# Kernel tuning notes

Measured on AMD Instinct MI355X. Metric: run time of the kernel, lower is better.

## Reference

```python
import jax, jax.numpy as jnp
import numpy as np

D = 768

def setup_inputs() -> dict:
    key = jax.random.key(0)
    k1, k2, k3, k4, k5 = jax.random.split(key, 5)
    B, C, Q = 32, 512, 128
    cont_embs = jax.random.normal(k1, (B, C, D), dtype=jnp.float32)
    ques_embs = jax.random.normal(k2, (B, Q, D), dtype=jnp.float32)
    cont_masks = jax.random.randint(k3, (B, C), 0, 2, dtype=jnp.int32)
    ques_masks = jax.random.randint(k4, (B, Q), 0, 2, dtype=jnp.int32)
    # S_W param, 'uniform' initializer (keras default: U[-0.05, 0.05])
    S_W = jax.random.uniform(k5, (3 * D,), dtype=jnp.float32, minval=-0.05, maxval=0.05)
    return {"cont_embs": cont_embs, "cont_masks": cont_masks,
            "ques_embs": ques_embs, "ques_masks": ques_masks, "S_W": S_W}

def reference(cont_embs, cont_masks, ques_embs, ques_masks, S_W):
    c, q = cont_embs, ques_embs          # (B,C,D), (B,Q,D)
    # Decompose reduce_sum(concat([c_tile, q_tile, c*q], -1) * S_W, -1)
    # into rank-1 bias terms + a single matmul (no (B,C,Q,3D) materialization).
    w1, w2, w3 = S_W[:D], S_W[D:2 * D], S_W[2 * D:]
    similarity = (jnp.einsum('bcd,d->bc', c, w1)[:, :, None]
                  + jnp.einsum('bqd,d->bq', q, w2)[:, None, :]
                  + jnp.einsum('bcd,bqd->bcq', c * w3, q))   # (B,C,Q)
    NEG = jnp.float32(-1e30)
    exp_mask_c2q = (1.0 - ques_masks.astype(jnp.float32))[:, None, :] * NEG  # (B,1,Q)
    # NOTE: original code applies softmax over axis=1 (context axis), faithfully kept.
    c2q_dist = jax.nn.softmax(similarity + exp_mask_c2q, axis=1)  # (B,C,Q)
    c2q = jnp.einsum('bcq,bqd->bcd', c2q_dist, q)                 # (B,C,D)
    S_max = jnp.max(similarity, axis=2)                           # (B,C)
    exp_mask_S = (1.0 - cont_masks.astype(jnp.float32)) * NEG     # (B,C)
    c_dash_dist = jax.nn.softmax(S_max + exp_mask_S, axis=1)      # (B,C)
    c_dash = jnp.einsum('bc,bcd->bd', c_dash_dist, c)[:, None, :] # (B,1,D)
    c_c2q = c * c2q
    c_c_dash = c * c_dash
    attn_output = jnp.concatenate([c2q, c_c2q, c_c_dash], axis=2)  # (B,C,3D)
    # dropout omitted (deterministic reference)
    blended_reps = jnp.concatenate([c, attn_output], axis=2)       # (B,C,4D)
    return blended_reps
```

## Files before the change

kernel.cpp:

```cpp
#include <hip/hip_runtime.h>
#include <hip/hip_bf16.h>

#define B_ 32
#define C_ 512
#define Q_ 128
#define D_ 768
constexpr float NEGV = -1e30f;
constexpr float CINV = 1.0f / 512.0f;

typedef short bf16x8 __attribute__((ext_vector_type(8)));
typedef short bf16x4 __attribute__((ext_vector_type(4)));
typedef float f32x4 __attribute__((ext_vector_type(4)));

__device__ __forceinline__ short f2bf(float x) {
    union { float f; unsigned u; } v; v.f = x;
    unsigned r = v.u + 0x7fffu + ((v.u >> 16) & 1u);
    return (short)(r >> 16);
}

__global__ void k_dots(const float* __restrict__ cont, const float* __restrict__ ques,
                       const float* __restrict__ SW, float* __restrict__ cdot,
                       float* __restrict__ qdot) {
    int w = threadIdx.x >> 6;
    int lane = threadIdx.x & 63;
    int r = blockIdx.x * 4 + w;
    const float* row;
    const float* wv;
    if (r < B_ * C_) { row = cont + (size_t)r * D_; wv = SW; }
    else             { row = ques + (size_t)(r - B_ * C_) * D_; wv = SW + D_; }
    float s = 0.f;
#pragma unroll
    for (int i = 0; i < D_ / 64; ++i) {
        int d = lane + i * 64;
        s += row[d] * wv[d];
    }
#pragma unroll
    for (int off = 32; off; off >>= 1) s += __shfl_xor(s, off, 64);
    if (lane == 0) {
        if (r < B_ * C_) cdot[r] = s;
        else qdot[r - B_ * C_] = s;
    }
}

__global__ void __launch_bounds__(512) k_sim(const float* __restrict__ cont,
                                             const float* __restrict__ ques,
                                             const float* __restrict__ SW,
                                             const float* __restrict__ cdot,
                                             const float* __restrict__ qdot,
                                             float* __restrict__ S,
                                             float* __restrict__ Smax) {
    const int b = blockIdx.y, c0 = blockIdx.x * 64;
    __shared__ short Alds[64 * 32];
    __shared__ short Blds[128 * 32];
    __shared__ float rowpart[4][64];
    char* Ab = (char*)Alds;
    char* Bb = (char*)Blds;
    const int t = threadIdx.x;
    const int w = t >> 6, l = t & 63;
    const int woffm = (w >> 2) * 32, woffn = (w & 3) * 32;
    const int lhi = l >> 4, llo = l & 15;
    f32x4 acc[2][2] = {};

    const int arow = t >> 3, akq = (t & 7) * 4;
    const int brow = t >> 2, bkq = (t & 3) * 8;
    const float* Ap = cont + ((size_t)(b * C_ + c0 + arow)) * D_ + akq;
    const float* Bp = ques + ((size_t)(b * Q_ + brow)) * D_ + bkq;
    const float* w3 = SW + 2 * D_;
    const int aoff = arow * 64 + ((((akq >> 3) ^ (arow & 3)) << 4) | ((akq & 4) << 1));
    const int boff = brow * 64 + (((bkq >> 3) ^ (brow & 3)) << 4);

    for (int k0 = 0; k0 < D_; k0 += 32) {
        float4 av = *(const float4*)(Ap + k0);
        float4 w4 = *(const float4*)(w3 + k0 + akq);
        bf16x4 a4;
        a4[0] = f2bf(av.x * w4.x); a4[1] = f2bf(av.y * w4.y);
        a4[2] = f2bf(av.z * w4.z); a4[3] = f2bf(av.w * w4.w);
        *(bf16x4*)(Ab + aoff) = a4;
        float4 b0 = *(const float4*)(Bp + k0);
        float4 b1 = *(const float4*)(Bp + k0 + 4);
        bf16x8 b8;
        b8[0] = f2bf(b0.x); b8[1] = f2bf(b0.y); b8[2] = f2bf(b0.z); b8[3] = f2bf(b0.w);
        b8[4] = f2bf(b1.x); b8[5] = f2bf(b1.y); b8[6] = f2bf(b1.z); b8[7] = f2bf(b1.w);
        *(bf16x8*)(Bb + boff) = b8;
        __syncthreads();
        bf16x8 af[2], bfv[2];
#pragma unroll
        for (int mi = 0; mi < 2; ++mi) {
            int row = woffm + mi * 16 + llo;
            af[mi] = *(bf16x8*)(Ab + row * 64 + ((lhi ^ (row & 3)) << 4));
        }
#pragma unroll
        for (int ni = 0; ni < 2; ++ni) {
            int row = woffn + ni * 16 + llo;
            bfv[ni] = *(bf16x8*)(Bb + row * 64 + ((lhi ^ (row & 3)) << 4));
        }
#pragma unroll
        for (int mi = 0; mi < 2; ++mi)
#pragma unroll
            for (int ni = 0; ni < 2; ++ni)
                acc[mi][ni] = __builtin_amdgcn_mfma_f32_16x16x32_bf16(af[mi], bfv[ni], acc[mi][ni], 0, 0, 0);
        __syncthreads();
    }

    float qd0 = qdot[b * Q_ + woffn + llo];
    float qd1 = qdot[b * Q_ + woffn + 16 + llo];
#pragma unroll
    for (int mi = 0; mi < 2; ++mi) {
#pragma unroll
        for (int i = 0; i < 4; ++i) {
            int cl = woffm + mi * 16 + lhi * 4 + i;
            float cd = cdot[b * C_ + c0 + cl];
            size_t srow = ((size_t)(b * C_ + c0 + cl)) * Q_;
            float v0 = acc[mi][0][i] + cd + qd0;
            float v1 = acc[mi][1][i] + cd + qd1;
            S[srow + woffn + llo] = v0;
            S[srow + woffn + 16 + llo] = v1;
            float vm = fmaxf(v0, v1);
#pragma unroll
            for (int off = 1; off < 16; off <<= 1) vm = fmaxf(vm, __shfl_xor(vm, off, 64));
            if (llo == 0) rowpart[w & 3][cl] = vm;
        }
    }
    __syncthreads();
    if (t < 64) {
        float m = fmaxf(fmaxf(rowpart[0][t], rowpart[1][t]), fmaxf(rowpart[2][t], rowpart[3][t]));
        Smax[b * C_ + c0 + t] = m;
    }
}

__global__ void k_colstats(const float* __restrict__ S, float* __restrict__ colM,
                           float* __restrict__ colInvL) {
    int b = blockIdx.y;
    int ql = threadIdx.x & 31;
    int q = blockIdx.x * 32 + ql;
    int strip = threadIdx.x >> 5;
    float m = -INFINITY, l = 0.f;
    const float* Sp = S + ((size_t)(b * C_ + strip * 64)) * Q_ + q;
    for (int c = 0; c < 64; ++c) {
        float v = Sp[(size_t)c * Q_];
        if (v > m) { l = l * __expf(m - v) + 1.f; m = v; }
        else l += __expf(v - m);
    }
    __shared__ float sm[8][32], sl[8][32];
    sm[strip][ql] = m; sl[strip][ql] = l;
    __syncthreads();
    if (threadIdx.x < 32) {
        float M = sm[0][ql], L = sl[0][ql];
#pragma unroll
        for (int i = 1; i < 8; ++i) {
            float mi = sm[i][ql], li = sl[i][ql];
            if (mi > M) { L = L * __expf(M - mi) + li; M = mi; }
            else L += li * __expf(mi - M);
        }
        colM[b * Q_ + q] = M;
        colInvL[b * Q_ + q] = 1.f / L;
    }
}

__global__ void k_cdash(const float* __restrict__ cont, const int* __restrict__ cmask,
                        const float* __restrict__ Smax, float* __restrict__ cdash) {
    int b = blockIdx.y, d0 = blockIdx.x * 64;
    __shared__ float dist[C_];
    __shared__ float red[256];
    __shared__ float ps[4][64];
    int t = threadIdx.x;
    float v0 = Smax[b * C_ + t]       + (cmask[b * C_ + t]       ? 0.f : NEGV);
    float v1 = Smax[b * C_ + t + 256] + (cmask[b * C_ + t + 256] ? 0.f : NEGV);
    float m = fmaxf(v0, v1);
    red[t] = m; __syncthreads();
    for (int s = 128; s; s >>= 1) { if (t < s) red[t] = fmaxf(red[t], red[t + s]); __syncthreads(); }
    m = red[0]; __syncthreads();
    float e0 = __expf(v0 - m), e1 = __expf(v1 - m);
    red[t] = e0 + e1; __syncthreads();
    for (int s = 128; s; s >>= 1) { if (t < s) red[t] += red[t + s]; __syncthreads(); }
    float inv = 1.f / red[0];
    dist[t] = e0 * inv; dist[t + 256] = e1 * inv;
    __syncthreads();
    int d = d0 + (t & 63), strip = t >> 6;
    float acc = 0.f;
    const float* cp = cont + ((size_t)(b * C_ + strip * 128)) * D_ + d;
#pragma unroll 4
    for (int c = 0; c < 128; ++c) acc += dist[strip * 128 + c] * cp[(size_t)c * D_];
    ps[strip][t & 63] = acc;
    __syncthreads();
    if (t < 64) cdash[b * D_ + d0 + t] = ps[0][t] + ps[1][t] + ps[2][t] + ps[3][t];
}

__global__ void __launch_bounds__(256) k_final(const float* __restrict__ cont,
                                               const float* __restrict__ ques,
                                               const int* __restrict__ qmask,
                                               const float* __restrict__ S,
                                               const float* __restrict__ colM,
                                               const float* __restrict__ colInvL,
                                               const float* __restrict__ cdash,
                                               float* __restrict__ out) {
    const int b = blockIdx.z, c0 = blockIdx.x * 64, D0 = blockIdx.y * 64;
    __shared__ short Alds[64 * 32];
    __shared__ short BldsT[64 * 32];
    __shared__ float colMl[Q_];
    __shared__ float scl[Q_];
    __shared__ float Cf[64][68];
    char* Ab = (char*)Alds;
    char* Bb = (char*)BldsT;
    const int t = threadIdx.x;
    const int w = t >> 6, l = t & 63;
    const int woffm = (w >> 1) * 32, woffn = (w & 1) * 32;
    const int lhi = l >> 4, llo = l & 15;
    f32x4 acc[2][2] = {};

    if (t < Q_) {
        colMl[t] = colM[b * Q_ + t];
        scl[t] = qmask[b * Q_ + t] ? colInvL[b * Q_ + t] : -1.f;
    }
    __syncthreads();

    const int arow = t >> 2, akq = (t & 3) * 8;
    const int qloc = t & 31, dgrp = t >> 5;
    const int aoff = arow * 64 + (((akq >> 3) ^ (arow & 3)) << 4);

    for (int kk = 0; kk < 4; ++kk) {
        const int q0 = kk * 32;
        {
            const float* sp = S + ((size_t)(b * C_ + c0 + arow)) * Q_ + q0 + akq;
            float4 s0 = *(const float4*)sp;
            float4 s1 = *(const float4*)(sp + 4);
            float sv[8] = {s0.x, s0.y, s0.z, s0.w, s1.x, s1.y, s1.z, s1.w};
            bf16x8 a8;
#pragma unroll
            for (int j = 0; j < 8; ++j) {
                int q = q0 + akq + j;
                float sc = scl[q];
                float dist = (sc < 0.f) ? CINV : __expf(sv[j] - colMl[q]) * sc;
                a8[j] = f2bf(dist);
            }
            *(bf16x8*)(Ab + aoff) = a8;
        }
        {
            const float* qp = ques + ((size_t)(b * Q_ + q0 + qloc)) * D_ + D0 + dgrp * 8;
            float4 b0 = *(const float4*)qp;
            float4 b1 = *(const float4*)(qp + 4);
            float bv[8] = {b0.x, b0.y, b0.z, b0.w, b1.x, b1.y, b1.z, b1.w};
#pragma unroll
            for (int j = 0; j < 8; ++j) {
                int d = dgrp * 8 + j;
                int byte = d * 64 + ((((qloc >> 3) ^ (d & 3)) << 4) | ((qloc & 7) * 2));
                *(short*)(Bb + byte) = f2bf(bv[j]);
            }
        }
        __syncthreads();
        bf16x8 af[2], bfv[2];
#pragma unroll
        for (int mi = 0; mi < 2; ++mi) {
            int row = woffm + mi * 16 + llo;
            af[mi] = *(bf16x8*)(Ab + row * 64 + ((lhi ^ (row & 3)) << 4));
        }
#pragma unroll
        for (int ni = 0; ni < 2; ++ni) {
            int row = woffn + ni * 16 + llo;
            bfv[ni] = *(bf16x8*)(Bb + row * 64 + ((lhi ^ (row & 3)) << 4));
        }
#pragma unroll
        for (int mi = 0; mi < 2; ++mi)
#pragma unroll
            for (int ni = 0; ni < 2; ++ni)
                acc[mi][ni] = __builtin_amdgcn_mfma_f32_16x16x32_bf16(af[mi], bfv[ni], acc[mi][ni], 0, 0, 0);
        __syncthreads();
    }

#pragma unroll
    for (int mi = 0; mi < 2; ++mi)
#pragma unroll
        for (int ni = 0; ni < 2; ++ni)
#pragma unroll
            for (int i = 0; i < 4; ++i)
                Cf[woffm + mi * 16 + lhi * 4 + i][woffn + ni * 16 + llo] = acc[mi][ni][i];
    __syncthreads();

    const int r = t >> 2, dch = (t & 3) * 16;
    const int cg = c0 + r;
    const float* cp = cont + ((size_t)(b * C_ + cg)) * D_ + D0 + dch;
    const float* dp = cdash + b * D_ + D0 + dch;
    float* op = out + ((size_t)(b * C_ + cg)) * (size_t)(4 * D_) + D0 + dch;
#pragma unroll
    for (int j = 0; j < 4; ++j) {
        float4 cv = *(const float4*)(cp + 4 * j);
        float4 av = *(const float4*)&Cf[r][dch + 4 * j];
        float4 dv = *(const float4*)(dp + 4 * j);
        float4 m1 = {cv.x * av.x, cv.y * av.y, cv.z * av.z, cv.w * av.w};
        float4 m2 = {cv.x * dv.x, cv.y * dv.y, cv.z * dv.z, cv.w * dv.w};
        *(float4*)(op + 4 * j) = cv;
        *(float4*)(op + D_ + 4 * j) = av;
        *(float4*)(op + 2 * D_ + 4 * j) = m1;
        *(float4*)(op + 3 * D_ + 4 * j) = m2;
    }
}

extern "C" void kernel_launch(void* const* d_in, const int* in_sizes, int n_in,
                              void* d_out, int out_size, void* d_ws, size_t ws_size,
                              hipStream_t stream) {
    const float* cont  = (const float*)d_in[0];
    const int*   cmask = (const int*)d_in[1];
    const float* ques  = (const float*)d_in[2];
    const int*   qmask = (const int*)d_in[3];
    const float* SW    = (const float*)d_in[4];
    float* out = (float*)d_out;

    float* ws      = (float*)d_ws;
    float* S       = ws;
    float* Smax    = S + (size_t)B_ * C_ * Q_;
    float* colM    = Smax + B_ * C_;
    float* colInvL = colM + B_ * Q_;
    float* cdot    = colInvL + B_ * Q_;
    float* qdot    = cdot + B_ * C_;
    float* cdash   = qdot + B_ * Q_;

    k_dots<<<(B_ * C_ + B_ * Q_) / 4, 256, 0, stream>>>(cont, ques, SW, cdot, qdot);
    k_sim<<<dim3(C_ / 64, B_), 512, 0, stream>>>(cont, ques, SW, cdot, qdot, S, Smax);
    k_colstats<<<dim3(Q_ / 32, B_), 256, 0, stream>>>(S, colM, colInvL);
    k_cdash<<<dim3(D_ / 64, B_), 256, 0, stream>>>(cont, cmask, Smax, cdash);
    k_final<<<dim3(C_ / 64, D_ / 64, B_), 256, 0, stream>>>(cont, ques, qmask, S, colM, colInvL, cdash, out);
}
```

Before: 358.4 us.

## Precompute bf16 operands and softmax dist, feed MFMA directly from global memory

Adds a prep kernel that writes a bf16 copy of cont*w3 and of ques while computing the rank-1 dots, a transpose kernel for ques, and a separate kernel that turns S into bf16 softmax weights. The sim and final GEMMs then load MFMA fragments straight from global memory, with no LDS staging, no conversions and no barriers in the K loop. Column stats and the sim kernel also use smaller blocks so more of them run at once. The aim is to stop redoing fp32-to-bf16 conversion and exp work in every tile, at the price of extra workspace traffic and more kernel launches.

New measurement: 322.2 us. -10.1%, faster.

```diff
diff --git a/kernel.cpp b/kernel.cpp
--- a/kernel.cpp
+++ b/kernel.cpp
@@ -18,143 +18,170 @@
     return (short)(r >> 16);
 }
 
-__global__ void k_dots(const float* __restrict__ cont, const float* __restrict__ ques,
-                       const float* __restrict__ SW, float* __restrict__ cdot,
+__global__ void k_prep(const float* __restrict__ cont, const float* __restrict__ ques,
+                       const float* __restrict__ SW, short* __restrict__ contw3,
+                       short* __restrict__ quesbf, float* __restrict__ cdot,
                        float* __restrict__ qdot) {
-    int w = threadIdx.x >> 6;
     int lane = threadIdx.x & 63;
-    int r = blockIdx.x * 4 + w;
-    const float* row;
-    const float* wv;
-    if (r < B_ * C_) { row = cont + (size_t)r * D_; wv = SW; }
-    else             { row = ques + (size_t)(r - B_ * C_) * D_; wv = SW + D_; }
-    float s = 0.f;
-#pragma unroll
-    for (int i = 0; i < D_ / 64; ++i) {
-        int d = lane + i * 64;
-        s += row[d] * wv[d];
-    }
-#pragma unroll
-    for (int off = 32; off; off >>= 1) s += __shfl_xor(s, off, 64);
-    if (lane == 0) {
-        if (r < B_ * C_) cdot[r] = s;
-        else qdot[r - B_ * C_] = s;
-    }
-}
-
-__global__ void __launch_bounds__(512) k_sim(const float* __restrict__ cont,
-                                             const float* __restrict__ ques,
-                                             const float* __restrict__ SW,
+    int r = blockIdx.x * 4 + (threadIdx.x >> 6);
+    float acc = 0.f;
+    if (r < B_ * C_) {
+        const float* row = cont + (size_t)r * D_;
+        short* orow = contw3 + (size_t)r * D_;
+#pragma unroll
+        for (int i = 0; i < 3; ++i) {
+            int k = i * 256 + lane * 4;
+            float4 f = *(const float4*)(row + k);
+            float4 a = *(const float4*)(SW + k);
+            float4 m = *(const float4*)(SW + 2 * D_ + k);
+            acc += f.x * a.x + f.y * a.y + f.z * a.z + f.w * a.w;
+            bf16x4 p;
+            p[0] = f2bf(f.x * m.x); p[1] = f2bf(f.y * m.y);
+            p[2] = f2bf(f.z * m.z); p[3] = f2bf(f.w * m.w);
+            *(bf16x4*)(orow + k) = p;
+        }
+#pragma unroll
+        for (int off = 32; off; off >>= 1) acc += __shfl_xor(acc, off, 64);
+        if (lane == 0) cdot[r] = acc;
+    } else {
+        int r2 = r - B_ * C_;
+        const float* row = ques + (size_t)r2 * D_;
+        short* orow = quesbf + (size_t)r2 * D_;
+#pragma unroll
+        for (int i = 0; i < 3; ++i) {
+            int k = i * 256 + lane * 4;
+            float4 f = *(const float4*)(row + k);
+            float4 a = *(const float4*)(SW + D_ + k);
+            acc += f.x * a.x + f.y * a.y + f.z * a.z + f.w * a.w;
+            bf16x4 p;
+            p[0] = f2bf(f.x); p[1] = f2bf(f.y); p[2] = f2bf(f.z); p[3] = f2bf(f.w);
+            *(bf16x4*)(orow + k) = p;
+        }
+#pragma unroll
+        for (int off = 32; off; off >>= 1) acc += __shfl_xor(acc, off, 64);
+        if (lane == 0) qdot[r2] = acc;
+    }
+}
+
+__global__ void k_qt(const short* __restrict__ quesbf, short* __restrict__ quesT) {
+    const int d0 = blockIdx.x * 64, q0 = blockIdx.y * 64, b = blockIdx.z;
+    __shared__ short T[64][65];
+    const int t = threadIdx.x;
+#pragma unroll
+    for (int p = 0; p < 2; ++p) {
+        int ql = p * 32 + (t >> 3), dl = (t & 7) * 8;
+        bf16x8 v = *(const bf16x8*)(quesbf + ((size_t)(b * Q_ + q0 + ql)) * D_ + d0 + dl);
+#pragma unroll
+        for (int j = 0; j < 8; ++j) T[ql][dl + j] = v[j];
+    }
+    __syncthreads();
+#pragma unroll
+    for (int p = 0; p < 2; ++p) {
+        int dl = p * 32 + (t >> 3), ql = (t & 7) * 8;
+        bf16x8 v;
+#pragma unroll
+        for (int j = 0; j < 8; ++j) v[j] = T[ql + j][dl];
+        *(bf16x8*)(quesT + ((size_t)(b * D_ + d0 + dl)) * Q_ + q0 + ql) = v;
+    }
+}
+
+__global__ void __launch_bounds__(256) k_sim(const short* __restrict__ contw3,
+                                             const short* __restrict__ quesbf,
                                              const float* __restrict__ cdot,
                                              const float* __restrict__ qdot,
                                              float* __restrict__ S,
                                              float* __restrict__ Smax) {
-    const int b = blockIdx.y, c0 = blockIdx.x * 64;
-    __shared__ short Alds[64 * 32];
-    __shared__ short Blds[128 * 32];
-    __shared__ float rowpart[4][64];
-    char* Ab = (char*)Alds;
-    char* Bb = (char*)Blds;
-    const int t = threadIdx.x;
-    const int w = t >> 6, l = t & 63;
-    const int woffm = (w >> 2) * 32, woffn = (w & 3) * 32;
-    const int lhi = l >> 4, llo = l & 15;
+    const int b = blockIdx.y, c0 = blockIdx.x * 32;
+    const int t = threadIdx.x, w = t >> 6, l = t & 63;
+    const int llo = l & 15, lhi = l >> 4;
+    __shared__ float rowpart[4][32];
+    const short* Ab = contw3 + ((size_t)(b * C_ + c0)) * D_ + lhi * 8;
+    const short* Bb = quesbf + ((size_t)(b * Q_ + w * 32)) * D_ + lhi * 8;
     f32x4 acc[2][2] = {};
-
-    const int arow = t >> 3, akq = (t & 7) * 4;
-    const int brow = t >> 2, bkq = (t & 3) * 8;
-    const float* Ap = cont + ((size_t)(b * C_ + c0 + arow)) * D_ + akq;
-    const float* Bp = ques + ((size_t)(b * Q_ + brow)) * D_ + bkq;
-    const float* w3 = SW + 2 * D_;
-    const int aoff = arow * 64 + ((((akq >> 3) ^ (arow & 3)) << 4) | ((akq & 4) << 1));
-    const int boff = brow * 64 + (((bkq >> 3) ^ (brow & 3)) << 4);
-
+#pragma unroll 4
     for (int k0 = 0; k0 < D_; k0 += 32) {
-        float4 av = *(const float4*)(Ap + k0);
-        float4 w4 = *(const float4*)(w3 + k0 + akq);
-        bf16x4 a4;
-        a4[0] = f2bf(av.x * w4.x); a4[1] = f2bf(av.y * w4.y);
-        a4[2] = f2bf(av.z * w4.z); a4[3] = f2bf(av.w * w4.w);
-        *(bf16x4*)(Ab + aoff) = a4;
-        float4 b0 = *(const float4*)(Bp + k0);
-        float4 b1 = *(const float4*)(Bp + k0 + 4);
-        bf16x8 b8;
-        b8[0] = f2bf(b0.x); b8[1] = f2bf(b0.y); b8[2] = f2bf(b0.z); b8[3] = f2bf(b0.w);
-        b8[4] = f2bf(b1.x); b8[5] = f2bf(b1.y); b8[6] = f2bf(b1.z); b8[7] = f2bf(b1.w);
-        *(bf16x8*)(Bb + boff) = b8;
-        __syncthreads();
-        bf16x8 af[2], bfv[2];
-#pragma unroll
-        for (int mi = 0; mi < 2; ++mi) {
-            int row = woffm + mi * 16 + llo;
-            af[mi] = *(bf16x8*)(Ab + row * 64 + ((lhi ^ (row & 3)) << 4));
-        }
-#pragma unroll
-        for (int ni = 0; ni < 2; ++ni) {
-            int row = woffn + ni * 16 + llo;
-            bfv[ni] = *(bf16x8*)(Bb + row * 64 + ((lhi ^ (row & 3)) << 4));
-        }
-#pragma unroll
-        for (int mi = 0; mi < 2; ++mi)
-#pragma unroll
-            for (int ni = 0; ni < 2; ++ni)
-                acc[mi][ni] = __builtin_amdgcn_mfma_f32_16x16x32_bf16(af[mi], bfv[ni], acc[mi][ni], 0, 0, 0);
-        __syncthreads();
-    }
-
-    float qd0 = qdot[b * Q_ + woffn + llo];
-    float qd1 = qdot[b * Q_ + woffn + 16 + llo];
+        bf16x8 a0 = *(const bf16x8*)(Ab + (size_t)llo * D_ + k0);
+        bf16x8 a1 = *(const bf16x8*)(Ab + (size_t)(16 + llo) * D_ + k0);
+        bf16x8 b0 = *(const bf16x8*)(Bb + (size_t)llo * D_ + k0);
+        bf16x8 b1 = *(const bf16x8*)(Bb + (size_t)(16 + llo) * D_ + k0);
+        acc[0][0] = __builtin_amdgcn_mfma_f32_16x16x32_bf16(a0, b0, acc[0][0], 0, 0, 0);
+        acc[0][1] = __builtin_amdgcn_mfma_f32_16x16x32_bf16(a0, b1, acc[0][1], 0, 0, 0);
+        acc[1][0] = __builtin_amdgcn_mfma_f32_16x16x32_bf16(a1, b0, acc[1][0], 0, 0, 0);
+        acc[1][1] = __builtin_amdgcn_mfma_f32_16x16x32_bf16(a1, b1, acc[1][1], 0, 0, 0);
+    }
+    float qd0 = qdot[b * Q_ + w * 32 + llo];
+    float qd1 = qdot[b * Q_ + w * 32 + 16 + llo];
 #pragma unroll
     for (int mi = 0; mi < 2; ++mi) {
 #pragma unroll
         for (int i = 0; i < 4; ++i) {
-            int cl = woffm + mi * 16 + lhi * 4 + i;
+            int cl = mi * 16 + lhi * 4 + i;
             float cd = cdot[b * C_ + c0 + cl];
             size_t srow = ((size_t)(b * C_ + c0 + cl)) * Q_;
             float v0 = acc[mi][0][i] + cd + qd0;
             float v1 = acc[mi][1][i] + cd + qd1;
-            S[srow + woffn + llo] = v0;
-            S[srow + woffn + 16 + llo] = v1;
+            S[srow + w * 32 + llo] = v0;
+            S[srow + w * 32 + 16 + llo] = v1;
             float vm = fmaxf(v0, v1);
 #pragma unroll
             for (int off = 1; off < 16; off <<= 1) vm = fmaxf(vm, __shfl_xor(vm, off, 64));
-            if (llo == 0) rowpart[w & 3][cl] = vm;
-        }
-    }
-    __syncthreads();
-    if (t < 64) {
-        float m = fmaxf(fmaxf(rowpart[0][t], rowpart[1][t]), fmaxf(rowpart[2][t], rowpart[3][t]));
-        Smax[b * C_ + c0 + t] = m;
-    }
-}
-
-__global__ void k_colstats(const float* __restrict__ S, float* __restrict__ colM,
-                           float* __restrict__ colInvL) {
-    int b = blockIdx.y;
-    int ql = threadIdx.x & 31;
-    int q = blockIdx.x * 32 + ql;
-    int strip = threadIdx.x >> 5;
-    float m = -INFINITY, l = 0.f;
-    const float* Sp = S + ((size_t)(b * C_ + strip * 64)) * Q_ + q;
-    for (int c = 0; c < 64; ++c) {
+            if (llo == 0) rowpart[w][cl] = vm;
+        }
+    }
+    __syncthreads();
+    if (t < 32)
+        Smax[b * C_ + c0 + t] = fmaxf(fmaxf(rowpart[0][t], rowpart[1][t]),
+                                      fmaxf(rowpart[2][t], rowpart[3][t]));
+}
+
+__global__ void k_colstats(const float* __restrict__ S, const int* __restrict__ qmask,
+                           float* __restrict__ colM, float* __restrict__ scl) {
+    const int b = blockIdx.y;
+    const int ql = threadIdx.x & 15, q = blockIdx.x * 16 + ql;
+    const int strip = threadIdx.x >> 4;
+    float m = -INFINITY, lsum = 0.f;
+    const float* Sp = S + ((size_t)(b * C_ + strip * 32)) * Q_ + q;
+    for (int c = 0; c < 32; ++c) {
         float v = Sp[(size_t)c * Q_];
-        if (v > m) { l = l * __expf(m - v) + 1.f; m = v; }
-        else l += __expf(v - m);
-    }
-    __shared__ float sm[8][32], sl[8][32];
-    sm[strip][ql] = m; sl[strip][ql] = l;
-    __syncthreads();
-    if (threadIdx.x < 32) {
+        if (v > m) { lsum = lsum * __expf(m - v) + 1.f; m = v; }
+        else lsum += __expf(v - m);
+    }
+    __shared__ float sm[16][16], sl[16][16];
+    sm[strip][ql] = m; sl[strip][ql] = lsum;
+    __syncthreads();
+    if (threadIdx.x < 16) {
         float M = sm[0][ql], L = sl[0][ql];
 #pragma unroll
-        for (int i = 1; i < 8; ++i) {
+        for (int i = 1; i < 16; ++i) {
             float mi = sm[i][ql], li = sl[i][ql];
             if (mi > M) { L = L * __expf(M - mi) + li; M = mi; }
             else L += li * __expf(mi - M);
         }
         colM[b * Q_ + q] = M;
-        colInvL[b * Q_ + q] = 1.f / L;
-    }
+        scl[b * Q_ + q] = qmask[b * Q_ + q] ? 1.f / L : -1.f;
+    }
+}
+
+__global__ void k_dist(const float* __restrict__ S, const float* __restrict__ colM,
+                       const float* __restrict__ scl, short* __restrict__ distbf) {
+    const int r = blockIdx.x * 16 + (threadIdx.x >> 4);
+    const int b = r >> 9;
+    const int q8 = (threadIdx.x & 15) * 8;
+    const float* sp = S + (size_t)r * Q_ + q8;
+    float4 s0 = *(const float4*)sp;
+    float4 s1 = *(const float4*)(sp + 4);
+    float4 m0 = *(const float4*)(colM + b * Q_ + q8);
+    float4 m1 = *(const float4*)(colM + b * Q_ + q8 + 4);
+    float4 c0 = *(const float4*)(scl + b * Q_ + q8);
+    float4 c1 = *(const float4*)(scl + b * Q_ + q8 + 4);
+    float sv[8] = {s0.x, s0.y, s0.z, s0.w, s1.x, s1.y, s1.z, s1.w};
+    float mv[8] = {m0.x, m0.y, m0.z, m0.w, m1.x, m1.y, m1.z, m1.w};
+    float cv[8] = {c0.x, c0.y, c0.z, c0.w, c1.x, c1.y, c1.z, c1.w};
+    bf16x8 o;
+#pragma unroll
+    for (int j = 0; j < 8; ++j)
+        o[j] = f2bf(cv[j] < 0.f ? CINV : __expf(sv[j] - mv[j]) * cv[j]);
+    *(bf16x8*)(distbf + (size_t)r * Q_ + q8) = o;
 }
 
 __global__ void k_cdash(const float* __restrict__ cont, const int* __restrict__ cmask,
@@ -179,7 +206,7 @@
     int d = d0 + (t & 63), strip = t >> 6;
     float acc = 0.f;
     const float* cp = cont + ((size_t)(b * C_ + strip * 128)) * D_ + d;
-#pragma unroll 4
+#pragma unroll 8
     for (int c = 0; c < 128; ++c) acc += dist[strip * 128 + c] * cp[(size_t)c * D_];
     ps[strip][t & 63] = acc;
     __syncthreads();
@@ -187,86 +214,30 @@
 }
 
 __global__ void __launch_bounds__(256) k_final(const float* __restrict__ cont,
-                                               const float* __restrict__ ques,
-                                               const int* __restrict__ qmask,
-                                               const float* __restrict__ S,
-                                               const float* __restrict__ colM,
-                                               const float* __restrict__ colInvL,
+                                               const short* __restrict__ distbf,
+                                               const short* __restrict__ quesT,
                                                const float* __restrict__ cdash,
                                                float* __restrict__ out) {
     const int b = blockIdx.z, c0 = blockIdx.x * 64, D0 = blockIdx.y * 64;
-    __shared__ short Alds[64 * 32];
-    __shared__ short BldsT[64 * 32];
-    __shared__ float colMl[Q_];
-    __shared__ float scl[Q_];
+    const int t = threadIdx.x, w = t >> 6, l = t & 63;
+    const int woffm = (w >> 1) * 32, woffn = (w & 1) * 32;
+    const int llo = l & 15, lhi = l >> 4;
     __shared__ float Cf[64][68];
-    char* Ab = (char*)Alds;
-    char* Bb = (char*)BldsT;
-    const int t = threadIdx.x;
-    const int w = t >> 6, l = t & 63;
-    const int woffm = (w >> 1) * 32, woffn = (w & 1) * 32;
-    const int lhi = l >> 4, llo = l & 15;
+    const short* Ab = distbf + ((size_t)(b * C_ + c0 + woffm)) * Q_ + lhi * 8;
+    const short* Bb = quesT + ((size_t)(b * D_ + D0 + woffn)) * Q_ + lhi * 8;
     f32x4 acc[2][2] = {};
-
-    if (t < Q_) {
-        colMl[t] = colM[b * Q_ + t];
-        scl[t] = qmask[b * Q_ + t] ? colInvL[b * Q_ + t] : -1.f;
-    }
-    __syncthreads();
-
-    const int arow = t >> 2, akq = (t & 3) * 8;
-    const int qloc = t & 31, dgrp = t >> 5;
-    const int aoff = arow * 64 + (((akq >> 3) ^ (arow & 3)) << 4);
-
+#pragma unroll
     for (int kk = 0; kk < 4; ++kk) {
-        const int q0 = kk * 32;
-        {
-            const float* sp = S + ((size_t)(b * C_ + c0 + arow)) * Q_ + q0 + akq;
-            float4 s0 = *(const float4*)sp;
-            float4 s1 = *(const float4*)(sp + 4);
-            float sv[8] = {s0.x, s0.y, s0.z, s0.w, s1.x, s1.y, s1.z, s1.w};
-            bf16x8 a8;
-#pragma unroll
-            for (int j = 0; j < 8; ++j) {
-                int q = q0 + akq + j;
-                float sc = scl[q];
-                float dist = (sc < 0.f) ? CINV : __expf(sv[j] - colMl[q]) * sc;
-                a8[j] = f2bf(dist);
-            }
-            *(bf16x8*)(Ab + aoff) = a8;
-        }
-        {
-            const float* qp = ques + ((size_t)(b * Q_ + q0 + qloc)) * D_ + D0 + dgrp * 8;
-            float4 b0 = *(const float4*)qp;
-            float4 b1 = *(const float4*)(qp + 4);
-            float bv[8] = {b0.x, b0.y, b0.z, b0.w, b1.x, b1.y, b1.z, b1.w};
-#pragma unroll
-            for (int j = 0; j < 8; ++j) {
-                int d = dgrp * 8 + j;
-                int byte = d * 64 + ((((qloc >> 3) ^ (d & 3)) << 4) | ((qloc & 7) * 2));
-                *(short*)(Bb + byte) = f2bf(bv[j]);
-            }
-        }
-        __syncthreads();
-        bf16x8 af[2], bfv[2];
-#pragma unroll
-        for (int mi = 0; mi < 2; ++mi) {
-            int row = woffm + mi * 16 + llo;
-            af[mi] = *(bf16x8*)(Ab + row * 64 + ((lhi ^ (row & 3)) << 4));
-        }
-#pragma unroll
-        for (int ni = 0; ni < 2; ++ni) {
-            int row = woffn + ni * 16 + llo;
-            bfv[ni] = *(bf16x8*)(Bb + row * 64 + ((lhi ^ (row & 3)) << 4));
-        }
-#pragma unroll
-        for (int mi = 0; mi < 2; ++mi)
-#pragma unroll
-            for (int ni = 0; ni < 2; ++ni)
-                acc[mi][ni] = __builtin_amdgcn_mfma_f32_16x16x32_bf16(af[mi], bfv[ni], acc[mi][ni], 0, 0, 0);
-        __syncthreads();
-    }
-
+        const int k0 = kk * 32;
+        bf16x8 a0 = *(const bf16x8*)(Ab + llo * Q_ + k0);
+        bf16x8 a1 = *(const bf16x8*)(Ab + (16 + llo) * Q_ + k0);
+        bf16x8 b0 = *(const bf16x8*)(Bb + llo * Q_ + k0);
+        bf16x8 b1 = *(const bf16x8*)(Bb + (16 + llo) * Q_ + k0);
+        acc[0][0] = __builtin_amdgcn_mfma_f32_16x16x32_bf16(a0, b0, acc[0][0], 0, 0, 0);
+        acc[0][1] = __builtin_amdgcn_mfma_f32_16x16x32_bf16(a0, b1, acc[0][1], 0, 0, 0);
+        acc[1][0] = __builtin_amdgcn_mfma_f32_16x16x32_bf16(a1, b0, acc[1][0], 0, 0, 0);
+        acc[1][1] = __builtin_amdgcn_mfma_f32_16x16x32_bf16(a1, b1, acc[1][1], 0, 0, 0);
+    }
 #pragma unroll
     for (int mi = 0; mi < 2; ++mi)
 #pragma unroll
@@ -275,23 +246,21 @@
             for (int i = 0; i < 4; ++i)
                 Cf[woffm + mi * 16 + lhi * 4 + i][woffn + ni * 16 + llo] = acc[mi][ni][i];
     __syncthreads();
-
-    const int r = t >> 2, dch = (t & 3) * 16;
-    const int cg = c0 + r;
-    const float* cp = cont + ((size_t)(b * C_ + cg)) * D_ + D0 + dch;
-    const float* dp = cdash + b * D_ + D0 + dch;
-    float* op = out + ((size_t)(b * C_ + cg)) * (size_t)(4 * D_) + D0 + dch;
-#pragma unroll
-    for (int j = 0; j < 4; ++j) {
-        float4 cv = *(const float4*)(cp + 4 * j);
-        float4 av = *(const float4*)&Cf[r][dch + 4 * j];
-        float4 dv = *(const float4*)(dp + 4 * j);
+    const int col = (t & 15) * 4;
+    const float4 dv = *(const float4*)(cdash + b * D_ + D0 + col);
+#pragma unroll
+    for (int p = 0; p < 4; ++p) {
+        int r = p * 16 + (t >> 4);
+        float4 av = *(const float4*)&Cf[r][col];
+        const float* cp = cont + ((size_t)(b * C_ + c0 + r)) * D_ + D0 + col;
+        float4 cv = *(const float4*)cp;
         float4 m1 = {cv.x * av.x, cv.y * av.y, cv.z * av.z, cv.w * av.w};
         float4 m2 = {cv.x * dv.x, cv.y * dv.y, cv.z * dv.z, cv.w * dv.w};
-        *(float4*)(op + 4 * j) = cv;
-        *(float4*)(op + D_ + 4 * j) = av;
-        *(float4*)(op + 2 * D_ + 4 * j) = m1;
-        *(float4*)(op + 3 * D_ + 4 * j) = m2;
+        float* op = out + ((size_t)(b * C_ + c0 + r)) * (size_t)(4 * D_) + D0 + col;
+        *(float4*)op = cv;
+        *(float4*)(op + D_) = av;
+        *(float4*)(op + 2 * D_) = m1;
+        *(float4*)(op + 3 * D_) = m2;
     }
 }
 
@@ -309,14 +278,20 @@
     float* S       = ws;
     float* Smax    = S + (size_t)B_ * C_ * Q_;
     float* colM    = Smax + B_ * C_;
-    float* colInvL = colM + B_ * Q_;
-    float* cdot    = colInvL + B_ * Q_;
+    float* scl     = colM + B_ * Q_;
+    float* cdot    = scl + B_ * Q_;
     float* qdot    = cdot + B_ * C_;
     float* cdash   = qdot + B_ * Q_;
-
-    k_dots<<<(B_ * C_ + B_ * Q_) / 4, 256, 0, stream>>>(cont, ques, SW, cdot, qdot);
-    k_sim<<<dim3(C_ / 64, B_), 512, 0, stream>>>(cont, ques, SW, cdot, qdot, S, Smax);
-    k_colstats<<<dim3(Q_ / 32, B_), 256, 0, stream>>>(S, colM, colInvL);
+    short* contw3  = (short*)(cdash + B_ * D_);
+    short* quesbf  = contw3 + (size_t)B_ * C_ * D_;
+    short* quesT   = quesbf + (size_t)B_ * Q_ * D_;
+    short* distbf  = quesT + (size_t)B_ * D_ * Q_;
+
+    k_prep<<<(B_ * C_ + B_ * Q_) / 4, 256, 0, stream>>>(cont, ques, SW, contw3, quesbf, cdot, qdot);
+    k_qt<<<dim3(D_ / 64, Q_ / 64, B_), 256, 0, stream>>>(quesbf, quesT);
+    k_sim<<<dim3(C_ / 32, B_), 256, 0, stream>>>(contw3, quesbf, cdot, qdot, S, Smax);
+    k_colstats<<<dim3(Q_ / 16, B_), 256, 0, stream>>>(S, qmask, colM, scl);
+    k_dist<<<B_ * C_ / 16, 256, 0, stream>>>(S, colM, scl, distbf);
     k_cdash<<<dim3(D_ / 64, B_), 256, 0, stream>>>(cont, cmask, Smax, cdash);
-    k_final<<<dim3(C_ / 64, D_ / 64, B_), 256, 0, stream>>>(cont, ques, qmask, S, colM, colInvL, cdash, out);
-}
+    k_final<<<dim3(C_ / 64, D_ / 64, B_), 256, 0, stream>>>(cont, distbf, quesT, cdash, out);
+}
```
